# Optimization experiments

Hardware: AMD Instinct MI355X
Metric: run time of the kernel (lower is better)

## Reference

```python
import jax, jax.numpy as jnp
import numpy as np

B, S, D, H = 2, 2048, 1024, 16  # batch, seq, rep_dim, num_heads
DH = D // H
MASK_VALUE = -1e-06  # value passed by MHAttention to masked_softmax (NOT -1e6)


def setup_inputs() -> dict:
    key = jax.random.key(0)
    ks = jax.random.split(key, 16)
    def xavier(k, shape):
        fan_in, fan_out = shape[0], shape[1]
        limit = float(np.sqrt(6.0 / (fan_in + fan_out)))
        return jax.random.uniform(k, shape, jnp.float32, -limit, limit)
    return {
        "queries": jax.random.normal(ks[0], (B, S, D), jnp.float32),
        "keys": jax.random.normal(ks[1], (B, S, D), jnp.float32),
        "values": jax.random.normal(ks[2], (B, S, D), jnp.float32),
        "thresholds": jax.random.randint(ks[3], (B,), 1, S + 1, jnp.int32),
        # Linear params stored as (in, out) so y = x @ W + b
        "Wq": xavier(ks[4], (D, D)), "bq": jnp.zeros((D,), jnp.float32),
        "Wk": xavier(ks[5], (D, D)), "bk": jnp.zeros((D,), jnp.float32),
        "Wv": xavier(ks[6], (D, D)), "bv": jnp.zeros((D,), jnp.float32),
        "W": xavier(ks[7], (DH, DH)),  # learnable bilinear attention matrix
        "Wo": xavier(ks[8], (D, D)), "bo": jnp.zeros((D,), jnp.float32),
    }


def reference(queries, keys, values, thresholds, Wq, bq, Wk, bk, Wv, bv, W, Wo, bo):
    def split_heads(x):  # (B,S,D) -> (B,H,S,DH)
        return x.reshape(B, S, H, DH).transpose(0, 2, 1, 3)

    Q = split_heads(queries @ Wq + bq)
    K = split_heads(keys @ Wk + bk)
    V = split_heads(values @ Wv + bv)

    # bilinear scores: (Q @ W) @ K^T, no 1/sqrt(d) scaling in original
    scores = jnp.einsum("bhqd,bhkd->bhqk", Q @ W, K)
    # mask key positions >= threshold[b] with MASK_VALUE before softmax
    keep = jnp.arange(S)[None, None, None, :] < thresholds[:, None, None, None]
    scores = jnp.where(keep, scores, MASK_VALUE)
    attn = jax.nn.softmax(scores, axis=-1)

    out = jnp.einsum("bhqk,bhkd->bhqd", attn, V)
    out = out.transpose(0, 2, 1, 3).reshape(B, S, D)  # merge heads
    return out @ Wo + bo
```

## Files before the change

### kernel.cpp

```cpp
#include <hip/hip_runtime.h>
#include <hip/hip_bf16.h>

#define D_MODEL 1024
#define NHEADS  16
#define DH      64
#define SEQ     2048
#define BATCH   2

#define LOG2E 1.4426950408889634f
#define MASKB2 (-1e-6f * LOG2E)
#define DEFER_THR 11.5456f
#define NEG_INF (-__builtin_inff())

typedef __attribute__((ext_vector_type(8))) short short8;
typedef __attribute__((ext_vector_type(4))) short short4v;
typedef __attribute__((ext_vector_type(4))) float f32x4;

#define AS1C(p) ((const __attribute__((address_space(1))) void*)(p))
#define AS3(p)  ((__attribute__((address_space(3))) void*)(p))

union PB { short4v s4; unsigned int u[2]; };

static __device__ __forceinline__ float fexp2(float x) {
    return __builtin_amdgcn_exp2f(x);
}

static __device__ __forceinline__ unsigned int pk2(float lo, float hi) {
    __hip_bfloat16 a = __float2bfloat16(lo), b = __float2bfloat16(hi);
    unsigned short au = *(unsigned short*)&a, bu = *(unsigned short*)&b;
    return (unsigned int)au | ((unsigned int)bu << 16);
}

__global__ __launch_bounds__(256) void prep_all_kernel(
    const float* __restrict__ Wq, const float* __restrict__ bq, const float* __restrict__ W,
    __hip_bfloat16* __restrict__ WqT, float* __restrict__ bq2,
    const float* __restrict__ Wk, const float* __restrict__ Wv, const float* __restrict__ Wo,
    __hip_bfloat16* __restrict__ WkT, __hip_bfloat16* __restrict__ WvT,
    __hip_bfloat16* __restrict__ WoT,
    const float* __restrict__ q, const float* __restrict__ k, const float* __restrict__ v,
    __hip_bfloat16* __restrict__ oq, __hip_bfloat16* __restrict__ ok,
    __hip_bfloat16* __restrict__ ov) {
    const int blk = blockIdx.x;
    const int t = threadIdx.x;

    if (blk < 1056) {
        const int c0 = (blk & 31) * 32;
        const int yy = blk >> 5;
        const int h = c0 >> 6, j0 = c0 & 63;
        if (yy == 32) {
            if (t < 32) {
                int col = c0 + t, j = col & 63;
                float s = 0.f;
#pragma unroll
                for (int d = 0; d < DH; ++d) s += bq[h * DH + d] * W[d * DH + j];
                bq2[col] = s * LOG2E;
            }
            return;
        }
        const int r0 = yy * 32;
        __shared__ float sWq[32][68];
        __shared__ float sW[64][36];
        __shared__ float sOut[32][33];
        {
            int lr = t >> 3, lc8 = (t & 7) * 8;
            const float* src = Wq + (size_t)(r0 + lr) * D_MODEL + h * DH + lc8;
            *(float4*)&sWq[lr][lc8]     = *(const float4*)(src);
            *(float4*)&sWq[lr][lc8 + 4] = *(const float4*)(src + 4);
            int d = t >> 2, c8 = (t & 3) * 8;
            const float* wsrc = W + (size_t)d * DH + j0 + c8;
            *(float4*)&sW[d][c8]     = *(const float4*)(wsrc);
            *(float4*)&sW[d][c8 + 4] = *(const float4*)(wsrc + 4);
        }
        __syncthreads();
        {
            int col_loc = t & 31, rq = t >> 5;
            float acc0 = 0.f, acc1 = 0.f, acc2 = 0.f, acc3 = 0.f;
#pragma unroll
            for (int d = 0; d < 64; ++d) {
                float wv = sW[d][col_loc];
                acc0 += sWq[rq * 4 + 0][d] * wv;
                acc1 += sWq[rq * 4 + 1][d] * wv;
                acc2 += sWq[rq * 4 + 2][d] * wv;
                acc3 += sWq[rq * 4 + 3][d] * wv;
            }
            sOut[col_loc][rq * 4 + 0] = acc0 * LOG2E;
            sOut[col_loc][rq * 4 + 1] = acc1 * LOG2E;
            sOut[col_loc][rq * 4 + 2] = acc2 * LOG2E;
            sOut[col_loc][rq * 4 + 3] = acc3 * LOG2E;
        }
        __syncthreads();
        {
            int orow = t >> 3, oc4 = (t & 7) * 4;
            __hip_bfloat16 o4[4];
#pragma unroll
            for (int i = 0; i < 4; ++i) o4[i] = __float2bfloat16(sOut[orow][oc4 + i]);
            *(short4*)(WqT + (size_t)(c0 + orow) * D_MODEL + r0 + oc4) = *(short4*)o4;
        }
    } else if (blk < 4128) {
        __shared__ float sT[32][33];
        int r = blk - 1056;
        int z = r >> 10; r &= 1023;
        const float* Win = (z == 0) ? Wk : (z == 1) ? Wv : Wo;
        __hip_bfloat16* Wt = (z == 0) ? WkT : (z == 1) ? WvT : WoT;
        int n0 = (r & 31) * 32, k0 = (r >> 5) * 32;
        int tx = t & 31, ty = t >> 5;
#pragma unroll
        for (int i = 0; i < 4; ++i)
            sT[ty + i * 8][tx] = Win[(size_t)(k0 + ty + i * 8) * D_MODEL + n0 + tx];
        __syncthreads();
#pragma unroll
        for (int i = 0; i < 4; ++i)
            Wt[(size_t)(n0 + ty + i * 8) * D_MODEL + k0 + tx] =
                __float2bfloat16(sT[tx][ty + i * 8]);
    } else {
        int idx = blk - 4128;
        int z = idx >> 11;
        int i = (idx & 2047) * 256 + t;
        const float* in = (z == 0) ? q : (z == 1) ? k : v;
        __hip_bfloat16* out = (z == 0) ? oq : (z == 1) ? ok : ov;
        float4 a = *(const float4*)(in + (size_t)i * 8);
        float4 b = *(const float4*)(in + (size_t)i * 8 + 4);
        __hip_bfloat16 o[8];
        o[0] = __float2bfloat16(a.x); o[1] = __float2bfloat16(a.y);
        o[2] = __float2bfloat16(a.z); o[3] = __float2bfloat16(a.w);
        o[4] = __float2bfloat16(b.x); o[5] = __float2bfloat16(b.y);
        o[6] = __float2bfloat16(b.z); o[7] = __float2bfloat16(b.w);
        *(short8*)(out + (size_t)i * 8) = *(short8*)o;
    }
}

#define GEMM_CORE(A_, BT_)                                                                  \
    __shared__ __hip_bfloat16 sA[2][128 * 32];                                              \
    __shared__ __hip_bfloat16 sB[2][128 * 32];                                              \
    const int t = threadIdx.x;                                                              \
    const int lane = t & 63, w = t >> 6;                                                    \
    const int g = lane >> 4, li = lane & 15;                                                \
    const int lin = blockIdx.y * 8 + blockIdx.x;                                            \
    const int ob = (lin & 7) * 32 + (lin >> 3);                                             \
    const int r0 = (ob >> 3) * 128, c0 = (ob & 7) * 128;                                    \
    const int wr = (w >> 1) * 64, wc = (w & 1) * 64;                                        \
    f32x4 acc[4][4] = {};                                                                   \
    auto stage = [&](int bb, int k0) {                                                      \
        _Pragma("unroll")                                                                   \
        for (int i = 0; i < 2; ++i) {                                                       \
            int o = (i * 4 + w) * 1024 + lane * 16;                                         \
            int row = o >> 6, ce = (o & 63) >> 1;                                           \
            __builtin_amdgcn_global_load_lds(AS1C(A_ + (size_t)(r0 + row) * 1024 + k0 + ce),\
                                             AS3((char*)sA[bb] + (i * 4 + w) * 1024), 16, 0, 0); \
            __builtin_amdgcn_global_load_lds(AS1C(BT_ + (size_t)(c0 + row) * 1024 + k0 + ce),\
                                             AS3((char*)sB[bb] + (i * 4 + w) * 1024), 16, 0, 0); \
        }                                                                                   \
    };                                                                                      \
    stage(0, 0);                                                                            \
    asm volatile("s_waitcnt vmcnt(0)" ::: "memory");                                        \
    __syncthreads();                                                                        \
    int cur = 0;                                                                            \
    for (int k0 = 0; k0 < 1024; k0 += 32) {                                                 \
        if (k0 + 32 < 1024) stage(cur ^ 1, k0 + 32);                                        \
        short8 af[4], bf[4];                                                                \
        _Pragma("unroll")                                                                   \
        for (int m = 0; m < 4; ++m)                                                         \
            af[m] = *(const short8*)(sA[cur] + (wr + m * 16 + li) * 32 + g * 8);            \
        _Pragma("unroll")                                                                   \
        for (int n = 0; n < 4; ++n)                                                         \
            bf[n] = *(const short8*)(sB[cur] + (wc + n * 16 + li) * 32 + g * 8);            \
        _Pragma("unroll")                                                                   \
        for (int m = 0; m < 4; ++m)                                                         \
            _Pragma("unroll")                                                               \
            for (int n = 0; n < 4; ++n)                                                     \
                acc[m][n] = __builtin_amdgcn_mfma_f32_16x16x32_bf16(af[m], bf[n], acc[m][n], 0, 0, 0); \
        asm volatile("s_waitcnt vmcnt(0)" ::: "memory");                                    \
        __syncthreads();                                                                    \
        cur ^= 1;                                                                           \
    }

__global__ __launch_bounds__(256) void gemm_qkv_kernel(
    const __hip_bfloat16* __restrict__ Xq, const __hip_bfloat16* __restrict__ Xk,
    const __hip_bfloat16* __restrict__ Xv,
    const __hip_bfloat16* __restrict__ WqT, const __hip_bfloat16* __restrict__ WkT,
    const __hip_bfloat16* __restrict__ WvT,
    const float* __restrict__ bq2, const float* __restrict__ bk, const float* __restrict__ bv,
    __hip_bfloat16* __restrict__ Qp, __hip_bfloat16* __restrict__ Kp,
    __hip_bfloat16* __restrict__ Vt) {
    const int z = blockIdx.z;
    const __hip_bfloat16* A  = (z == 0) ? Xq  : (z == 1) ? Xk  : Xv;
    const __hip_bfloat16* BT = (z == 0) ? WqT : (z == 1) ? WkT : WvT;
    const float* bias        = (z == 0) ? bq2 : (z == 1) ? bk  : bv;
    __hip_bfloat16* C        = (z == 0) ? Qp  : (z == 1) ? Kp  : Vt;

    GEMM_CORE(A, BT)

#pragma unroll
    for (int m = 0; m < 4; ++m) {
#pragma unroll
        for (int n = 0; n < 4; ++n) {
            int col = c0 + wc + n * 16 + li;
            float bs = bias[col];
            int row0 = r0 + wr + m * 16 + g * 4;
            int h = col >> 6, d = col & 63;
            if (z == 2) {
                int b = row0 >> 11, s0 = row0 & 2047;
                __hip_bfloat16 o4[4];
#pragma unroll
                for (int r = 0; r < 4; ++r) o4[r] = __float2bfloat16(acc[m][n][r] + bs);
                *(short4*)(C + (((size_t)(b * NHEADS + h)) * DH + d) * SEQ + s0) = *(short4*)o4;
            } else {
#pragma unroll
                for (int r = 0; r < 4; ++r) {
                    int row = row0 + r;
                    int b = row >> 11, s = row & 2047;
                    C[(((size_t)(b * NHEADS + h)) * SEQ + s) * DH + d] =
                        __float2bfloat16(acc[m][n][r] + bs);
                }
            }
        }
    }
}

__global__ __launch_bounds__(256) void gemm_out_kernel(
    const __hip_bfloat16* __restrict__ A, const __hip_bfloat16* __restrict__ BT,
    const float* __restrict__ bias, float* __restrict__ C) {
    GEMM_CORE(A, BT)
#pragma unroll
    for (int m = 0; m < 4; ++m) {
#pragma unroll
        for (int n = 0; n < 4; ++n) {
            int col = c0 + wc + n * 16 + li;
            float bs = bias[col];
            int row0 = r0 + wr + m * 16 + g * 4;
#pragma unroll
            for (int r = 0; r < 4; ++r)
                C[(size_t)(row0 + r) * D_MODEL + col] = acc[m][n][r] + bs;
        }
    }
}

__global__ __launch_bounds__(256) void vsum_kernel(const __hip_bfloat16* __restrict__ Vt,
                                                   const int* __restrict__ thresholds,
                                                   float* __restrict__ Vsum) {
    int bh = blockIdx.x, b = bh >> 4;
    int thresh = thresholds[b];
    int loop_end = min(SEQ, ((thresh + 63) >> 6) << 6);
    int t = threadIdx.x;
    int dh = t >> 2, sub = t & 3;
    const __hip_bfloat16* row = Vt + ((size_t)bh * DH + dh) * SEQ;
    float s = 0.f;
    for (int s0 = loop_end + sub * 8; s0 < SEQ; s0 += 32) {
        short8 v = *(const short8*)(row + s0);
#pragma unroll
        for (int j = 0; j < 8; ++j) {
            unsigned short us = (unsigned short)v[j];
            s += __bfloat162float(*(__hip_bfloat16*)&us);
        }
    }
    s += __shfl_xor(s, 1);
    s += __shfl_xor(s, 2);
    if (sub == 0) Vsum[bh * DH + dh] = s;
}

__global__ __launch_bounds__(256) void attn_mfma_kernel(
    const __hip_bfloat16* __restrict__ Qp,
    const __hip_bfloat16* __restrict__ Kp,
    const __hip_bfloat16* __restrict__ Vt,
    const int* __restrict__ thresholds,
    const float* __restrict__ Vsum,
    __hip_bfloat16* __restrict__ AO) {
    __shared__ char lds[32768];
    char* sK  = lds;
    char* sVT = lds + 16384;

    const int t = threadIdx.x, lane = t & 63, w = t >> 6;
    const int g = lane >> 4, li = lane & 15;
    const int bh = blockIdx.x, b = bh >> 4, h = bh & 15;
    const int q0 = blockIdx.y * 64;
    const int thresh = thresholds[b];
    const int loop_end = min(SEQ, ((thresh + 63) >> 6) << 6);
    const __hip_bfloat16* Qb = Qp + (size_t)bh * SEQ * DH;
    const __hip_bfloat16* Kb = Kp + (size_t)bh * SEQ * DH;
    const __hip_bfloat16* Vb = Vt + (size_t)bh * DH * SEQ;

    short8 qf[2];
#pragma unroll
    for (int kb = 0; kb < 2; ++kb)
        qf[kb] = *(const short8*)(Qb + (size_t)(q0 + w * 16 + li) * DH + kb * 32 + g * 8);

    f32x4 Oacc[4] = {};
    float mrun = NEG_INF, lpart = 0.f;

    auto stageK = [&](int bb, int kv) {
#pragma unroll
        for (int i = 0; i < 2; ++i) {
            int o = i * 4096 + w * 1024 + lane * 16;
            int key = o >> 7, slot = (o & 127) >> 4;
            __builtin_amdgcn_global_load_lds(
                AS1C(Kb + (size_t)(kv + key) * DH + ((slot ^ (key & 7)) << 3)),
                AS3(sK + bb * 8192 + i * 4096 + w * 1024), 16, 0, 0);
        }
    };
    auto stageV = [&](int bb, int kv) {
#pragma unroll
        for (int i = 0; i < 2; ++i) {
            int o = i * 4096 + w * 1024 + lane * 16;
            int dh = o >> 7, slot = (o & 127) >> 4;
            __builtin_amdgcn_global_load_lds(
                AS1C(Vb + (size_t)dh * SEQ + kv + ((slot ^ (dh & 7)) << 3)),
                AS3(sVT + bb * 8192 + i * 4096 + w * 1024), 16, 0, 0);
        }
    };

    stageK(0, 0); stageV(0, 0);
    asm volatile("s_waitcnt vmcnt(0)" ::: "memory");
    __syncthreads();

    int cur = 0;
    for (int kv0 = 0; kv0 < loop_end; kv0 += 64) {
        int nxt = kv0 + 64;
        if (nxt < loop_end) { stageK(cur ^ 1, nxt); stageV(cur ^ 1, nxt); }

        f32x4 S[4] = {};
        __builtin_amdgcn_s_setprio(1);
#pragma unroll
        for (int kb = 0; kb < 2; ++kb) {
            short8 kf[4];
#pragma unroll
            for (int n = 0; n < 4; ++n) {
                int key = 16 * n + li;
                kf[n] = *(const short8*)(sK + cur * 8192 + key * 128 +
                                         (((4 * kb + g) ^ (key & 7)) << 4));
            }
#pragma unroll
            for (int n = 0; n < 4; ++n)
                S[n] = __builtin_amdgcn_mfma_f32_16x16x32_bf16(kf[n], qf[kb], S[n], 0, 0, 0);
        }
        __builtin_amdgcn_s_setprio(0);

        if (kv0 + 64 > thresh) {
            int tr = thresh - kv0 - 4 * g;
#pragma unroll
            for (int n = 0; n < 4; ++n)
#pragma unroll
                for (int rr = 0; rr < 4; ++rr)
                    if (16 * n + rr >= tr) S[n][rr] = MASKB2;
        }

        float mx = S[0][0];
#pragma unroll
        for (int n = 0; n < 4; ++n)
#pragma unroll
            for (int rr = 0; rr < 4; ++rr) mx = fmaxf(mx, S[n][rr]);
        mx = fmaxf(mx, __shfl_xor(mx, 16));
        mx = fmaxf(mx, __shfl_xor(mx, 32));
        float pmax = mx;

        if (__any(pmax > mrun + DEFER_THR)) {
            float mn = fmaxf(mrun, pmax);
            float alpha = fexp2(mrun - mn);
            lpart *= alpha;
#pragma unroll
            for (int n = 0; n < 4; ++n)
#pragma unroll
                for (int rr = 0; rr < 4; ++rr) Oacc[n][rr] *= alpha;
            mrun = mn;
        }

        short4v pb[4];
#pragma unroll
        for (int n = 0; n < 4; ++n) {
#pragma unroll
            for (int rr = 0; rr < 4; ++rr) {
                float p = fexp2(S[n][rr] - mrun);
                S[n][rr] = p;
                lpart += p;
            }
            PB u;
            u.u[0] = pk2(S[n][0], S[n][1]);
            u.u[1] = pk2(S[n][2], S[n][3]);
            pb[n] = u.s4;
        }

        __builtin_amdgcn_s_setprio(1);
#pragma unroll
        for (int ks = 0; ks < 4; ++ks) {
            int slot = 2 * ks + (g >> 1);
            int sub8 = 8 * (g & 1);
#pragma unroll
            for (int n = 0; n < 4; ++n) {
                int dh = 16 * n + li;
                short4v va = *(const short4v*)(sVT + cur * 8192 + dh * 128 +
                                               ((slot ^ (dh & 7)) << 4) + sub8);
                Oacc[n] = __builtin_amdgcn_mfma_f32_16x16x16bf16_1k(va, pb[ks], Oacc[n], 0, 0, 0);
            }
        }
        __builtin_amdgcn_s_setprio(0);

        asm volatile("s_waitcnt vmcnt(0)" ::: "memory");
        __syncthreads();
        cur ^= 1;
    }

    float lrun = lpart;
    lrun += __shfl_xor(lrun, 16);
    lrun += __shfl_xor(lrun, 32);

    int nmask = SEQ - loop_end;
    if (nmask > 0) {
        const float* vs = Vsum + bh * DH;
        f32x4 vsf[4];
#pragma unroll
        for (int n = 0; n < 4; ++n) vsf[n] = *(const f32x4*)(vs + 16 * n + 4 * g);
        float pu = fexp2(MASKB2 - mrun);
        lrun += (float)nmask * pu;
#pragma unroll
        for (int n = 0; n < 4; ++n)
#pragma unroll
            for (int rr = 0; rr < 4; ++rr) Oacc[n][rr] += pu * vsf[n][rr];
    }

    float linv = 1.0f / lrun;
    int q = q0 + w * 16 + li;
#pragma unroll
    for (int n = 0; n < 4; ++n) {
        __hip_bfloat16 o4[4];
#pragma unroll
        for (int rr = 0; rr < 4; ++rr) o4[rr] = __float2bfloat16(Oacc[n][rr] * linv);
        *(short4*)(AO + (size_t)(b * SEQ + q) * D_MODEL + h * DH + 16 * n + 4 * g) =
            *(short4*)o4;
    }
}

extern "C" void kernel_launch(void* const* d_in, const int* in_sizes, int n_in,
                              void* d_out, int out_size, void* d_ws, size_t ws_size,
                              hipStream_t stream) {
    const float* queries    = (const float*)d_in[0];
    const float* keys       = (const float*)d_in[1];
    const float* values     = (const float*)d_in[2];
    const int*   thresholds = (const int*)d_in[3];
    const float* Wq = (const float*)d_in[4];
    const float* bq = (const float*)d_in[5];
    const float* Wk = (const float*)d_in[6];
    const float* bk = (const float*)d_in[7];
    const float* Wv = (const float*)d_in[8];
    const float* bv = (const float*)d_in[9];
    const float* W  = (const float*)d_in[10];
    const float* Wo = (const float*)d_in[11];
    const float* bo = (const float*)d_in[12];
    float* out = (float*)d_out;

    char* wsb = (char*)d_ws;
    float* bq2  = (float*)wsb;
    float* Vsum = (float*)(wsb + 4096);
    __hip_bfloat16* XqB = (__hip_bfloat16*)(wsb + 16384);
    __hip_bfloat16* XkB = XqB + (1 << 22);
    __hip_bfloat16* XvB = XkB + (1 << 22);
    __hip_bfloat16* WqT = XvB + (1 << 22);
    __hip_bfloat16* WkT = WqT + (1 << 20);
    __hip_bfloat16* WvT = WkT + (1 << 20);
    __hip_bfloat16* WoT = WvT + (1 << 20);
    __hip_bfloat16* QpB = WoT + (1 << 20);
    __hip_bfloat16* KpB = QpB + (1 << 22);
    __hip_bfloat16* VtB = KpB + (1 << 22);
    __hip_bfloat16* AOB = XqB;

    prep_all_kernel<<<10272, 256, 0, stream>>>(Wq, bq, W, WqT, bq2,
                                               Wk, Wv, Wo, WkT, WvT, WoT,
                                               queries, keys, values, XqB, XkB, XvB);

    gemm_qkv_kernel<<<dim3(8, 32, 3), 256, 0, stream>>>(XqB, XkB, XvB, WqT, WkT, WvT,
                                                        bq2, bk, bv, QpB, KpB, VtB);
    vsum_kernel<<<32, 256, 0, stream>>>(VtB, thresholds, Vsum);

    attn_mfma_kernel<<<dim3(32, 32), 256, 0, stream>>>(QpB, KpB, VtB, thresholds, Vsum, AOB);

    gemm_out_kernel<<<dim3(8, 32), 256, 0, stream>>>(AOB, WoT, bo, out);
}
```

Measured before the change: 151.8 us.

## Split attention KV loop across two blocks and merge with a combine kernel

Splits each attention block's key/value tile range into two halves handled by separate blocks (grid z=2). Each block writes unnormalized bf16 partial outputs plus per-row max and sum. A new combine kernel rescales and merges the halves into the attention output. The aim is more parallelism and shorter per-block serial loops, since 1024 blocks with data-dependent loop lengths may underfill the GPU. The cost is an extra launch, extra partial-output traffic, and bf16 rounding of the unnormalized partials. WqT is reused to hold the max/sum buffers; this is safe only because the Q projection has already consumed WqT before attention runs.

New measurement: 157.9 us. +4.0%, slower.

```diff
diff --git a/kernel.cpp b/kernel.cpp
--- a/kernel.cpp
+++ b/kernel.cpp
@@ -29,6 +29,11 @@
     __hip_bfloat16 a = __float2bfloat16(lo), b = __float2bfloat16(hi);
     unsigned short au = *(unsigned short*)&a, bu = *(unsigned short*)&b;
     return (unsigned int)au | ((unsigned int)bu << 16);
+}
+
+static __device__ __forceinline__ float bf2f(short s) {
+    unsigned int u = ((unsigned int)(unsigned short)s) << 16;
+    return *(float*)&u;
 }
 
 __global__ __launch_bounds__(256) void prep_all_kernel(
@@ -264,17 +269,24 @@
     const __hip_bfloat16* __restrict__ Vt,
     const int* __restrict__ thresholds,
     const float* __restrict__ Vsum,
-    __hip_bfloat16* __restrict__ AO) {
+    __hip_bfloat16* __restrict__ Opart,
+    float* __restrict__ Mpart,
+    float* __restrict__ Lpart) {
     __shared__ char lds[32768];
     char* sK  = lds;
     char* sVT = lds + 16384;
 
     const int t = threadIdx.x, lane = t & 63, w = t >> 6;
     const int g = lane >> 4, li = lane & 15;
-    const int bh = blockIdx.x, b = bh >> 4, h = bh & 15;
+    const int bh = blockIdx.x, b = bh >> 4;
     const int q0 = blockIdx.y * 64;
+    const int z = blockIdx.z;
     const int thresh = thresholds[b];
     const int loop_end = min(SEQ, ((thresh + 63) >> 6) << 6);
+    const int nt = loop_end >> 6;
+    const int nth = (nt + 1) >> 1;
+    const int t0 = (z == 0) ? 0 : nth;
+    const int t1 = (z == 0) ? nth : nt;
     const __hip_bfloat16* Qb = Qp + (size_t)bh * SEQ * DH;
     const __hip_bfloat16* Kb = Kp + (size_t)bh * SEQ * DH;
     const __hip_bfloat16* Vb = Vt + (size_t)bh * DH * SEQ;
@@ -308,121 +320,173 @@
         }
     };
 
-    stageK(0, 0); stageV(0, 0);
-    asm volatile("s_waitcnt vmcnt(0)" ::: "memory");
-    __syncthreads();
-
-    int cur = 0;
-    for (int kv0 = 0; kv0 < loop_end; kv0 += 64) {
-        int nxt = kv0 + 64;
-        if (nxt < loop_end) { stageK(cur ^ 1, nxt); stageV(cur ^ 1, nxt); }
-
-        f32x4 S[4] = {};
-        __builtin_amdgcn_s_setprio(1);
-#pragma unroll
-        for (int kb = 0; kb < 2; ++kb) {
-            short8 kf[4];
+    if (t0 < t1) {
+        stageK(0, t0 << 6); stageV(0, t0 << 6);
+        asm volatile("s_waitcnt vmcnt(0)" ::: "memory");
+        __syncthreads();
+
+        int cur = 0;
+        for (int tt = t0; tt < t1; ++tt) {
+            const int kv0 = tt << 6;
+            if (tt + 1 < t1) { stageK(cur ^ 1, kv0 + 64); stageV(cur ^ 1, kv0 + 64); }
+
+            f32x4 S[4] = {};
+            __builtin_amdgcn_s_setprio(1);
+#pragma unroll
+            for (int kb = 0; kb < 2; ++kb) {
+                short8 kf[4];
+#pragma unroll
+                for (int n = 0; n < 4; ++n) {
+                    int key = 16 * n + li;
+                    kf[n] = *(const short8*)(sK + cur * 8192 + key * 128 +
+                                             (((4 * kb + g) ^ (key & 7)) << 4));
+                }
+#pragma unroll
+                for (int n = 0; n < 4; ++n)
+                    S[n] = __builtin_amdgcn_mfma_f32_16x16x32_bf16(kf[n], qf[kb], S[n], 0, 0, 0);
+            }
+            __builtin_amdgcn_s_setprio(0);
+
+            if (kv0 + 64 > thresh) {
+                int tr = thresh - kv0 - 4 * g;
+#pragma unroll
+                for (int n = 0; n < 4; ++n)
+#pragma unroll
+                    for (int rr = 0; rr < 4; ++rr)
+                        if (16 * n + rr >= tr) S[n][rr] = MASKB2;
+            }
+
+            float mx = S[0][0];
+#pragma unroll
+            for (int n = 0; n < 4; ++n)
+#pragma unroll
+                for (int rr = 0; rr < 4; ++rr) mx = fmaxf(mx, S[n][rr]);
+            mx = fmaxf(mx, __shfl_xor(mx, 16));
+            mx = fmaxf(mx, __shfl_xor(mx, 32));
+            float pmax = mx;
+
+            if (__any(pmax > mrun + DEFER_THR)) {
+                float mn = fmaxf(mrun, pmax);
+                float alpha = fexp2(mrun - mn);
+                lpart *= alpha;
+#pragma unroll
+                for (int n = 0; n < 4; ++n)
+#pragma unroll
+                    for (int rr = 0; rr < 4; ++rr) Oacc[n][rr] *= alpha;
+                mrun = mn;
+            }
+
+            short4v pb[4];
 #pragma unroll
             for (int n = 0; n < 4; ++n) {
-                int key = 16 * n + li;
-                kf[n] = *(const short8*)(sK + cur * 8192 + key * 128 +
-                                         (((4 * kb + g) ^ (key & 7)) << 4));
-            }
-#pragma unroll
-            for (int n = 0; n < 4; ++n)
-                S[n] = __builtin_amdgcn_mfma_f32_16x16x32_bf16(kf[n], qf[kb], S[n], 0, 0, 0);
-        }
-        __builtin_amdgcn_s_setprio(0);
-
-        if (kv0 + 64 > thresh) {
-            int tr = thresh - kv0 - 4 * g;
-#pragma unroll
-            for (int n = 0; n < 4; ++n)
-#pragma unroll
-                for (int rr = 0; rr < 4; ++rr)
-                    if (16 * n + rr >= tr) S[n][rr] = MASKB2;
-        }
-
-        float mx = S[0][0];
-#pragma unroll
-        for (int n = 0; n < 4; ++n)
-#pragma unroll
-            for (int rr = 0; rr < 4; ++rr) mx = fmaxf(mx, S[n][rr]);
-        mx = fmaxf(mx, __shfl_xor(mx, 16));
-        mx = fmaxf(mx, __shfl_xor(mx, 32));
-        float pmax = mx;
-
-        if (__any(pmax > mrun + DEFER_THR)) {
-            float mn = fmaxf(mrun, pmax);
+#pragma unroll
+                for (int rr = 0; rr < 4; ++rr) {
+                    float p = fexp2(S[n][rr] - mrun);
+                    S[n][rr] = p;
+                    lpart += p;
+                }
+                PB u;
+                u.u[0] = pk2(S[n][0], S[n][1]);
+                u.u[1] = pk2(S[n][2], S[n][3]);
+                pb[n] = u.s4;
+            }
+
+            __builtin_amdgcn_s_setprio(1);
+#pragma unroll
+            for (int ks = 0; ks < 4; ++ks) {
+                int slot = 2 * ks + (g >> 1);
+                int sub8 = 8 * (g & 1);
+#pragma unroll
+                for (int n = 0; n < 4; ++n) {
+                    int dh = 16 * n + li;
+                    short4v va = *(const short4v*)(sVT + cur * 8192 + dh * 128 +
+                                                   ((slot ^ (dh & 7)) << 4) + sub8);
+                    Oacc[n] = __builtin_amdgcn_mfma_f32_16x16x16bf16_1k(va, pb[ks], Oacc[n], 0, 0, 0);
+                }
+            }
+            __builtin_amdgcn_s_setprio(0);
+
+            asm volatile("s_waitcnt vmcnt(0)" ::: "memory");
+            __syncthreads();
+            cur ^= 1;
+        }
+    }
+
+    float lrow = lpart;
+    lrow += __shfl_xor(lrow, 16);
+    lrow += __shfl_xor(lrow, 32);
+
+    if (z == 1) {
+        int nmask = SEQ - loop_end;
+        if (nmask > 0) {
+            float mn = fmaxf(mrun, MASKB2);
             float alpha = fexp2(mrun - mn);
-            lpart *= alpha;
+            lrow *= alpha;
 #pragma unroll
             for (int n = 0; n < 4; ++n)
 #pragma unroll
                 for (int rr = 0; rr < 4; ++rr) Oacc[n][rr] *= alpha;
             mrun = mn;
-        }
-
-        short4v pb[4];
-#pragma unroll
-        for (int n = 0; n < 4; ++n) {
-#pragma unroll
-            for (int rr = 0; rr < 4; ++rr) {
-                float p = fexp2(S[n][rr] - mrun);
-                S[n][rr] = p;
-                lpart += p;
-            }
-            PB u;
-            u.u[0] = pk2(S[n][0], S[n][1]);
-            u.u[1] = pk2(S[n][2], S[n][3]);
-            pb[n] = u.s4;
-        }
-
-        __builtin_amdgcn_s_setprio(1);
-#pragma unroll
-        for (int ks = 0; ks < 4; ++ks) {
-            int slot = 2 * ks + (g >> 1);
-            int sub8 = 8 * (g & 1);
-#pragma unroll
-            for (int n = 0; n < 4; ++n) {
-                int dh = 16 * n + li;
-                short4v va = *(const short4v*)(sVT + cur * 8192 + dh * 128 +
-                                               ((slot ^ (dh & 7)) << 4) + sub8);
-                Oacc[n] = __builtin_amdgcn_mfma_f32_16x16x16bf16_1k(va, pb[ks], Oacc[n], 0, 0, 0);
-            }
-        }
-        __builtin_amdgcn_s_setprio(0);
-
-        asm volatile("s_waitcnt vmcnt(0)" ::: "memory");
-        __syncthreads();
-        cur ^= 1;
-    }
-
-    float lrun = lpart;
-    lrun += __shfl_xor(lrun, 16);
-    lrun += __shfl_xor(lrun, 32);
-
-    int nmask = SEQ - loop_end;
-    if (nmask > 0) {
-        const float* vs = Vsum + bh * DH;
-        f32x4 vsf[4];
-#pragma unroll
-        for (int n = 0; n < 4; ++n) vsf[n] = *(const f32x4*)(vs + 16 * n + 4 * g);
-        float pu = fexp2(MASKB2 - mrun);
-        lrun += (float)nmask * pu;
-#pragma unroll
-        for (int n = 0; n < 4; ++n)
-#pragma unroll
-            for (int rr = 0; rr < 4; ++rr) Oacc[n][rr] += pu * vsf[n][rr];
-    }
-
-    float linv = 1.0f / lrun;
-    int q = q0 + w * 16 + li;
+            const float* vs = Vsum + bh * DH;
+            f32x4 vsf[4];
+#pragma unroll
+            for (int n = 0; n < 4; ++n) vsf[n] = *(const f32x4*)(vs + 16 * n + 4 * g);
+            float pu = fexp2(MASKB2 - mrun);
+            lrow += (float)nmask * pu;
+#pragma unroll
+            for (int n = 0; n < 4; ++n)
+#pragma unroll
+                for (int rr = 0; rr < 4; ++rr) Oacc[n][rr] += pu * vsf[n][rr];
+        }
+    }
+
+    const int blkid = (bh * 32 + blockIdx.y) * 2 + z;
+    if (g == 0) {
+        Mpart[blkid * 64 + w * 16 + li] = mrun;
+        Lpart[blkid * 64 + w * 16 + li] = lrow;
+    }
+    __hip_bfloat16* ob = Opart + (size_t)blkid * 4096 + t * 16;
 #pragma unroll
     for (int n = 0; n < 4; ++n) {
         __hip_bfloat16 o4[4];
 #pragma unroll
-        for (int rr = 0; rr < 4; ++rr) o4[rr] = __float2bfloat16(Oacc[n][rr] * linv);
+        for (int rr = 0; rr < 4; ++rr) o4[rr] = __float2bfloat16(Oacc[n][rr]);
+        *(short4*)(ob + n * 4) = *(short4*)o4;
+    }
+}
+
+__global__ __launch_bounds__(256) void attn_combine_kernel(
+    const __hip_bfloat16* __restrict__ Opart,
+    const float* __restrict__ Mpart,
+    const float* __restrict__ Lpart,
+    __hip_bfloat16* __restrict__ AO) {
+    const int t = threadIdx.x, lane = t & 63, w = t >> 6;
+    const int g = lane >> 4, li = lane & 15;
+    const int blkid2 = blockIdx.x;
+    const int bh = blkid2 >> 5, qb = blkid2 & 31;
+    const int b = bh >> 4, h = bh & 15;
+    const int ql = w * 16 + li;
+    const int base0 = blkid2 * 2, base1 = base0 + 1;
+
+    float m0 = Mpart[base0 * 64 + ql], m1 = Mpart[base1 * 64 + ql];
+    float l0 = Lpart[base0 * 64 + ql], l1 = Lpart[base1 * 64 + ql];
+    float m = fmaxf(m0, m1);
+    float a0 = fexp2(m0 - m), a1 = fexp2(m1 - m);
+    float linv = 1.0f / (l0 * a0 + l1 * a1);
+    float s0 = a0 * linv, s1 = a1 * linv;
+
+    const __hip_bfloat16* p0 = Opart + (size_t)base0 * 4096 + t * 16;
+    const __hip_bfloat16* p1 = Opart + (size_t)base1 * 4096 + t * 16;
+    int q = qb * 64 + ql;
+#pragma unroll
+    for (int n = 0; n < 4; ++n) {
+        short4 v0 = *(const short4*)(p0 + n * 4);
+        short4 v1 = *(const short4*)(p1 + n * 4);
+        __hip_bfloat16 o4[4];
+        o4[0] = __float2bfloat16(bf2f(v0.x) * s0 + bf2f(v1.x) * s1);
+        o4[1] = __float2bfloat16(bf2f(v0.y) * s0 + bf2f(v1.y) * s1);
+        o4[2] = __float2bfloat16(bf2f(v0.z) * s0 + bf2f(v1.z) * s1);
+        o4[3] = __float2bfloat16(bf2f(v0.w) * s0 + bf2f(v1.w) * s1);
         *(short4*)(AO + (size_t)(b * SEQ + q) * D_MODEL + h * DH + 16 * n + 4 * g) =
             *(short4*)o4;
     }
@@ -461,6 +525,10 @@
     __hip_bfloat16* VtB = KpB + (1 << 22);
     __hip_bfloat16* AOB = XqB;
 
+    __hip_bfloat16* Opart = XkB;
+    float* Mpart = (float*)WqT;
+    float* Lpart = Mpart + 2048 * 64;
+
     prep_all_kernel<<<10272, 256, 0, stream>>>(Wq, bq, W, WqT, bq2,
                                                Wk, Wv, Wo, WkT, WvT, WoT,
                                                queries, keys, values, XqB, XkB, XvB);
@@ -469,7 +537,9 @@
                                                         bq2, bk, bv, QpB, KpB, VtB);
     vsum_kernel<<<32, 256, 0, stream>>>(VtB, thresholds, Vsum);
 
-    attn_mfma_kernel<<<dim3(32, 32), 256, 0, stream>>>(QpB, KpB, VtB, thresholds, Vsum, AOB);
+    attn_mfma_kernel<<<dim3(32, 32, 2), 256, 0, stream>>>(QpB, KpB, VtB, thresholds, Vsum,
+                                                          Opart, Mpart, Lpart);
+    attn_combine_kernel<<<1024, 256, 0, stream>>>(Opart, Mpart, Lpart, AOB);
 
     gemm_out_kernel<<<dim3(8, 32), 256, 0, stream>>>(AOB, WoT, bo, out);
 }
```
